# Performance work log

Hardware: AMD Instinct MI355X
Metric: run time of the kernel (lower is better)

The kernel has to match this reference:

```python
import jax, jax.numpy as jnp
import numpy as np

DIM = 1024
NUM_HEADS = 16
HEAD_DIM = DIM // NUM_HEADS
SCALE = HEAD_DIM ** -0.5


def setup_inputs() -> dict:
    key = jax.random.key(0)
    ks = jax.random.split(key, 10)
    B, N, C = 8, 2048, DIM
    std = C ** -0.5
    return {
        "query": jax.random.normal(ks[0], (B, N, C), jnp.float32),
        "key": jax.random.normal(ks[1], (B, N, C), jnp.float32),
        "value": jax.random.normal(ks[2], (B, N, C), jnp.float32),
        "xpos": jax.random.randint(ks[3], (B, N, 2), 0, 64),
        "ypos": jax.random.randint(ks[4], (B, N, 2), 0, 64),
        # Linear weights stored [out, in] like torch; qkv_bias=False so no q/k/v bias.
        "Wq": jax.random.normal(ks[5], (C, C), jnp.float32) * std,
        "Wk": jax.random.normal(ks[6], (C, C), jnp.float32) * std,
        "Wv": jax.random.normal(ks[7], (C, C), jnp.float32) * std,
        "Wp": jax.random.normal(ks[8], (C, C), jnp.float32) * std,
        "bp": jax.random.normal(ks[9], (C,), jnp.float32) * std,
    }


def reference(query, key, value, xpos, ypos, Wq, Wk, Wv, Wp, bp):
    B, N, C = query.shape
    H, D = NUM_HEADS, HEAD_DIM
    # Separate Q/K/V projections (no bias), reshape to (B, N, H, D).
    q = (query @ Wq.T).reshape(B, N, H, D)
    k = (key @ Wk.T).reshape(B, N, H, D)
    v = (value @ Wv.T).reshape(B, N, H, D)
    # rope is None in this config, so no rotary embedding is applied.
    # Faithful to the source: NO permute before q @ k^T, so the contraction is
    # over D with attention logits of shape (B, N, H, H) (softmax over heads).
    attn = jnp.einsum("bnhd,bngd->bnhg", q, k) * SCALE
    attn = jax.nn.softmax(attn, axis=-1)
    x = jnp.einsum("bnhg,bngd->bnhd", attn, v)  # (B, N, H, D)
    # torch: (attn @ v).transpose(1, 2).reshape(B, N, C)
    x = jnp.transpose(x, (0, 2, 1, 3)).reshape(B, N, C)
    # Output projection (has bias); dropouts are p=0 / eval -> identity.
    return x @ Wp.T + bp
```

## Files before the change

kernel.cpp:

```cpp
#include <hip/hip_runtime.h>
#include <stdint.h>

#define DEV __device__ __forceinline__

using f32x4 = __attribute__((ext_vector_type(4))) float;
using s16x8 = __attribute__((ext_vector_type(8))) short;

DEV uint16_t f2bf(float f) {
  union { float f; uint32_t u; } v; v.f = f;
  uint32_t r = v.u + 0x7fffu + ((v.u >> 16) & 1u);
  return (uint16_t)(r >> 16);
}
DEV uint32_t pack2(float a, float b) {
  return (uint32_t)f2bf(a) | ((uint32_t)f2bf(b) << 16);
}

DEV void gload_lds16(const void* g, void* l) {
  __builtin_amdgcn_global_load_lds(
      (__attribute__((address_space(1))) void*)(void*)g,
      (__attribute__((address_space(3))) void*)l, 16, 0, 0);
}

__global__ __launch_bounds__(256) void cvt_all_kernel(
    const float* __restrict__ q, const float* __restrict__ k,
    const float* __restrict__ v, const float* __restrict__ Wq,
    const float* __restrict__ Wk, const float* __restrict__ Wv,
    const float* __restrict__ Wp, uint16_t* __restrict__ qc,
    uint16_t* __restrict__ kc, uint16_t* __restrict__ vc,
    uint16_t* __restrict__ wqb, uint16_t* __restrict__ wkb,
    uint16_t* __restrict__ wvb, uint16_t* __restrict__ wpb) {
  const int idx = blockIdx.x * blockDim.x + threadIdx.x;
  const float* src;
  uint16_t* dst;
  int i;
  if (idx < 3 * 2097152) {
    const int t = idx >> 21;
    i = idx & 2097151;
    src = t == 0 ? q : t == 1 ? k : v;
    dst = t == 0 ? qc : t == 1 ? kc : vc;
  } else {
    const int j = idx - 3 * 2097152;
    const int r = j >> 17;
    i = j & 131071;
    src = r == 0 ? Wq : r == 1 ? Wk : r == 2 ? Wv : Wp;
    dst = r == 0 ? wqb : r == 1 ? wkb : r == 2 ? wvb : wpb;
  }
  const float4* s = (const float4*)src;
  float4 a = s[2 * i];
  float4 b = s[2 * i + 1];
  uint4 pk;
  pk.x = pack2(a.x, a.y);
  pk.y = pack2(a.z, a.w);
  pk.z = pack2(b.x, b.y);
  pk.w = pack2(b.z, b.w);
  ((uint4*)dst)[i] = pk;
}

struct GemmBatch {
  const uint16_t* A[3];
  const uint16_t* B[3];
  void* C[3];
};

template <bool OUT_BF16>
__global__ __launch_bounds__(512, 2) void gemm_bt256(GemmBatch gb,
                                                     const float* __restrict__ bias,
                                                     int M, int N, int K) {
  constexpr int BM = 256, BN = 256, BK = 32;
  __shared__ __align__(16) uint16_t Alds[4][BM * BK];
  __shared__ __align__(16) uint16_t Blds[4][BN * BK];

  const int w = blockIdx.x;
  const int xcd = w & 7;
  int local = w >> 3;
  const int nbn = N >> 8;
  const int bmpx = (M >> 8) >> 3;
  const int bn = local % nbn;
  local /= nbn;
  const int bml = local % bmpx;
  const int z = local / bmpx;
  const int bm0 = (xcd * bmpx + bml) * BM;
  const int bn0 = bn * BN;

  const uint16_t* __restrict__ Ap = gb.A[z];
  const uint16_t* __restrict__ Bp = gb.B[z];
  void* __restrict__ Cp = gb.C[z];

  const int tid = threadIdx.x;
  const int wave = tid >> 6;
  const int lane = tid & 63;
  const int quad = lane >> 4;
  const int l16 = lane & 15;
  const int wm = (wave >> 2) * 128;
  const int wn = (wave & 3) * 64;

  f32x4 acc[8][4];
#pragma unroll
  for (int i = 0; i < 8; ++i)
#pragma unroll
    for (int j = 0; j < 4; ++j) acc[i][j] = (f32x4){0.f, 0.f, 0.f, 0.f};

  const uint16_t* asrc[2];
  const uint16_t* bsrc[2];
  int sofs[2];
#pragma unroll
  for (int j = 0; j < 2; ++j) {
    const int p = wave * 128 + j * 64 + lane;
    const int m = p >> 2;
    const int c = p & 3;
    const int lc = c ^ ((m >> 1) & 3);
    asrc[j] = Ap + (size_t)(bm0 + m) * K + lc * 8;
    bsrc[j] = Bp + (size_t)(bn0 + m) * K + lc * 8;
    sofs[j] = (wave * 128 + j * 64) * 8;
  }

  const int NT = K >> 5;

#pragma unroll
  for (int tt = 0; tt < 3; ++tt) {
#pragma unroll
    for (int j = 0; j < 2; ++j) gload_lds16(asrc[j] + tt * BK, &Alds[tt][sofs[j]]);
#pragma unroll
    for (int j = 0; j < 2; ++j) gload_lds16(bsrc[j] + tt * BK, &Blds[tt][sofs[j]]);
  }

  for (int t = 0; t < NT; ++t) {
    const int buf = t & 3;
    if (t + 2 < NT) {
      asm volatile("s_waitcnt vmcnt(8)" ::: "memory");
    } else if (t + 1 < NT) {
      asm volatile("s_waitcnt vmcnt(4)" ::: "memory");
    } else {
      asm volatile("s_waitcnt vmcnt(0)" ::: "memory");
    }
    __builtin_amdgcn_s_barrier();
    __builtin_amdgcn_sched_barrier(0);

    if (t + 3 < NT) {
      const int sb = (t + 3) & 3;
      const int ko = (t + 3) * BK;
#pragma unroll
      for (int j = 0; j < 2; ++j) gload_lds16(asrc[j] + ko, &Alds[sb][sofs[j]]);
#pragma unroll
      for (int j = 0; j < 2; ++j) gload_lds16(bsrc[j] + ko, &Blds[sb][sofs[j]]);
    }

    s16x8 bf[4];
#pragma unroll
    for (int nf = 0; nf < 4; ++nf) {
      const int nl = wn + nf * 16 + l16;
      const int cb = nl * 4 + (quad ^ ((nl >> 1) & 3));
      bf[nf] = *(const s16x8*)&Blds[buf][cb * 8];
    }

#pragma unroll
    for (int ph = 0; ph < 4; ++ph) {
      const int ml0 = wm + (ph * 2) * 16 + l16;
      const int ca0 = ml0 * 4 + (quad ^ ((ml0 >> 1) & 3));
      s16x8 af0 = *(const s16x8*)&Alds[buf][ca0 * 8];
      const int ml1 = wm + (ph * 2 + 1) * 16 + l16;
      const int ca1 = ml1 * 4 + (quad ^ ((ml1 >> 1) & 3));
      s16x8 af1 = *(const s16x8*)&Alds[buf][ca1 * 8];
      __builtin_amdgcn_s_setprio(1);
#pragma unroll
      for (int nf = 0; nf < 4; ++nf) {
        acc[ph * 2][nf] =
            __builtin_amdgcn_mfma_f32_16x16x32_bf16(af0, bf[nf], acc[ph * 2][nf], 0, 0, 0);
        acc[ph * 2 + 1][nf] =
            __builtin_amdgcn_mfma_f32_16x16x32_bf16(af1, bf[nf], acc[ph * 2 + 1][nf], 0, 0, 0);
      }
      __builtin_amdgcn_s_setprio(0);
    }
  }

#pragma unroll
  for (int sm = 0; sm < 8; ++sm) {
    const int mrow = bm0 + wm + sm * 16 + quad * 4;
#pragma unroll
    for (int sn = 0; sn < 4; ++sn) {
      const int ncol = bn0 + wn + sn * 16 + l16;
      if constexpr (OUT_BF16) {
        uint16_t* Cb = (uint16_t*)Cp;
#pragma unroll
        for (int r = 0; r < 4; ++r) Cb[(size_t)(mrow + r) * N + ncol] = f2bf(acc[sm][sn][r]);
      } else {
        float* Cf = (float*)Cp;
        const float bv = bias[ncol];
#pragma unroll
        for (int r = 0; r < 4; ++r) Cf[(size_t)(mrow + r) * N + ncol] = acc[sm][sn][r] + bv;
      }
    }
  }
}

__global__ __launch_bounds__(256) void attn_kernel(const uint16_t* __restrict__ qb,
                                                   const uint16_t* __restrict__ kb,
                                                   const uint16_t* __restrict__ vb,
                                                   uint16_t* __restrict__ x2b) {
  __shared__ __align__(16) uint16_t plds[4][16 * 16];
  __shared__ __align__(16) uint16_t vlds[4][16 * 64];

  const int tid = threadIdx.x;
  const int wave = tid >> 6;
  const int lane = tid & 63;
  const int quad = lane >> 4;
  const int l16 = lane & 15;
  const int token = blockIdx.x * 4 + wave;
  const int b = token >> 11;
  const int n = token & 2047;
  const size_t base = (size_t)token * 1024;

  {
    const uint16_t* vt = vb + base;
    uint16_t* vl = vlds[wave];
#pragma unroll
    for (int c2 = 0; c2 < 2; ++c2) {
      const int p = lane + c2 * 64;
      const int g = p >> 3;
      const int cc = p & 7;
      const int cs = cc ^ (2 * (g >> 3));
      *(uint4*)&vl[g * 64 + cs * 8] = *(const uint4*)&vt[p * 8];
    }
  }

  const uint16_t* qrow = qb + base + l16 * 64 + quad * 8;
  const uint16_t* krow = kb + base + l16 * 64 + quad * 8;
  s16x8 aq0 = *(const s16x8*)qrow;
  s16x8 aq1 = *(const s16x8*)(qrow + 32);
  s16x8 bk0 = *(const s16x8*)krow;
  s16x8 bk1 = *(const s16x8*)(krow + 32);
  f32x4 s = (f32x4){0.f, 0.f, 0.f, 0.f};
  s = __builtin_amdgcn_mfma_f32_16x16x32_bf16(aq0, bk0, s, 0, 0, 0);
  s = __builtin_amdgcn_mfma_f32_16x16x32_bf16(aq1, bk1, s, 0, 0, 0);

  float p[4];
#pragma unroll
  for (int r = 0; r < 4; ++r) {
    float v = s[r] * 0.125f;
    float mx = v;
#pragma unroll
    for (int off = 1; off < 16; off <<= 1) mx = fmaxf(mx, __shfl_xor(mx, off));
    float e = __expf(v - mx);
    float sum = e;
#pragma unroll
    for (int off = 1; off < 16; off <<= 1) sum += __shfl_xor(sum, off);
    p[r] = e / sum;
  }

  uint16_t* pb = plds[wave];
#pragma unroll
  for (int r = 0; r < 4; ++r) pb[(quad * 4 + r) * 16 + l16] = f2bf(p[r]);
  __syncthreads();
  s16x8 ap = (s16x8){0, 0, 0, 0, 0, 0, 0, 0};
  if (quad < 2) ap = *(const s16x8*)&pb[l16 * 16 + quad * 8];

  s16x8 bv[4];
#pragma unroll
  for (int c = 0; c < 4; ++c) bv[c] = (s16x8){0, 0, 0, 0, 0, 0, 0, 0};
  if (quad < 2) {
    const uint16_t* vl = vlds[wave];
#pragma unroll
    for (int c = 0; c < 4; ++c) {
      const int cc = c * 2 + (l16 >> 3);
      const int dlo = l16 & 7;
#pragma unroll
      for (int j = 0; j < 8; ++j) {
        const int g = quad * 8 + j;
        const int cs = cc ^ (2 * (g >> 3));
        bv[c][j] = (short)vl[g * 64 + cs * 8 + dlo];
      }
    }
  }

  f32x4 xacc[4];
#pragma unroll
  for (int c = 0; c < 4; ++c) {
    xacc[c] = (f32x4){0.f, 0.f, 0.f, 0.f};
    xacc[c] = __builtin_amdgcn_mfma_f32_16x16x32_bf16(ap, bv[c], xacc[c], 0, 0, 0);
  }

  uint16_t* xout =
      x2b + (size_t)b * (2048 * 1024) + (size_t)(n & 15) * 64 + (size_t)(n >> 4) * 1024;
#pragma unroll
  for (int c = 0; c < 4; ++c) {
    const int d = c * 16 + l16;
#pragma unroll
    for (int r = 0; r < 4; ++r) {
      const int h = quad * 4 + r;
      xout[(size_t)h * 128 * 1024 + d] = f2bf(xacc[c][r]);
    }
  }
}

extern "C" void kernel_launch(void* const* d_in, const int* in_sizes, int n_in,
                              void* d_out, int out_size, void* d_ws, size_t ws_size,
                              hipStream_t stream) {
  const float* query = (const float*)d_in[0];
  const float* key = (const float*)d_in[1];
  const float* value = (const float*)d_in[2];
  const float* Wq = (const float*)d_in[5];
  const float* Wk = (const float*)d_in[6];
  const float* Wv = (const float*)d_in[7];
  const float* Wp = (const float*)d_in[8];
  const float* bp = (const float*)d_in[9];
  float* out = (float*)d_out;

  const int C = 1024;
  const int M = 8 * 2048;
  const size_t MC = (size_t)M * C;
  const size_t CC = (size_t)C * C;

  uint16_t* ws = (uint16_t*)d_ws;
  uint16_t* qb = ws;
  uint16_t* kb = qb + MC;
  uint16_t* vb = kb + MC;
  uint16_t* x2b = vb + MC;
  uint16_t* wqb = x2b + MC;
  uint16_t* wkb = wqb + CC;
  uint16_t* wvb = wkb + CC;
  uint16_t* wpb = wvb + CC;
  uint16_t* kin = wpb + CC;
  uint16_t* vin = kin + MC;
  uint16_t* qin = x2b;

  cvt_all_kernel<<<dim3(26624), dim3(256), 0, stream>>>(
      query, key, value, Wq, Wk, Wv, Wp, qin, kin, vin, wqb, wkb, wvb, wpb);

  GemmBatch qkv;
  qkv.A[0] = qin;  qkv.B[0] = wqb;  qkv.C[0] = qb;
  qkv.A[1] = kin;  qkv.B[1] = wkb;  qkv.C[1] = kb;
  qkv.A[2] = vin;  qkv.B[2] = wvb;  qkv.C[2] = vb;
  gemm_bt256<true><<<dim3((M / 256) * (C / 256) * 3), dim3(512), 0, stream>>>(
      qkv, nullptr, M, C, C);

  attn_kernel<<<dim3(M / 4), dim3(256), 0, stream>>>(qb, kb, vb, x2b);

  GemmBatch fin;
  fin.A[0] = x2b;  fin.B[0] = wpb;  fin.C[0] = out;
  fin.A[1] = x2b;  fin.B[1] = wpb;  fin.C[1] = out;
  fin.A[2] = x2b;  fin.B[2] = wpb;  fin.C[2] = out;
  gemm_bt256<false><<<dim3((M / 256) * (C / 256)), dim3(512), 0, stream>>>(fin, bp, M,
                                                                           C, C);
}
```

Measured before the change: 428.8 us.

## Restructure GEMM into BK=64 double-buffered eight-phase pipelined schedule

Replaces the 4-stage BK=32 GEMM mainloop with a double-buffered BK=64 loop. Each K tile is split into four sub-phases that interleave LDS fragment loads, global-to-LDS prefetch of half-tiles, and MFMA blocks, each phase bracketed by barriers. The aim is to overlap global loads, LDS reads and matrix math more finely and to halve the number of K iterations. In exchange it adds many more barriers per tile, and the larger tile (128KB of LDS) may limit occupancy under the requested two blocks per CU.

Measured after the change: 392.4 us. 8.5% less time.

```diff
diff --git a/kernel.cpp b/kernel.cpp
--- a/kernel.cpp
+++ b/kernel.cpp
@@ -63,12 +63,12 @@
 };
 
 template <bool OUT_BF16>
-__global__ __launch_bounds__(512, 2) void gemm_bt256(GemmBatch gb,
-                                                     const float* __restrict__ bias,
-                                                     int M, int N, int K) {
-  constexpr int BM = 256, BN = 256, BK = 32;
-  __shared__ __align__(16) uint16_t Alds[4][BM * BK];
-  __shared__ __align__(16) uint16_t Blds[4][BN * BK];
+__global__ __launch_bounds__(512, 2) void gemm8p(GemmBatch gb,
+                                                 const float* __restrict__ bias,
+                                                 int M, int N, int K) {
+  constexpr int BM = 256, BN = 256, BK = 64;
+  __shared__ __align__(16) uint16_t Alds[2][BM * BK];
+  __shared__ __align__(16) uint16_t Blds[2][BN * BK];
 
   const int w = blockIdx.x;
   const int xcd = w & 7;
@@ -100,77 +100,116 @@
 #pragma unroll
     for (int j = 0; j < 4; ++j) acc[i][j] = (f32x4){0.f, 0.f, 0.f, 0.f};
 
-  const uint16_t* asrc[2];
-  const uint16_t* bsrc[2];
-  int sofs[2];
-#pragma unroll
-  for (int j = 0; j < 2; ++j) {
-    const int p = wave * 128 + j * 64 + lane;
-    const int m = p >> 2;
-    const int c = p & 3;
-    const int lc = c ^ ((m >> 1) & 3);
-    asrc[j] = Ap + (size_t)(bm0 + m) * K + lc * 8;
-    bsrc[j] = Bp + (size_t)(bn0 + m) * K + lc * 8;
-    sofs[j] = (wave * 128 + j * 64) * 8;
-  }
-
-  const int NT = K >> 5;
-
-#pragma unroll
-  for (int tt = 0; tt < 3; ++tt) {
-#pragma unroll
-    for (int j = 0; j < 2; ++j) gload_lds16(asrc[j] + tt * BK, &Alds[tt][sofs[j]]);
-#pragma unroll
-    for (int j = 0; j < 2; ++j) gload_lds16(bsrc[j] + tt * BK, &Blds[tt][sofs[j]]);
-  }
-
-  for (int t = 0; t < NT; ++t) {
-    const int buf = t & 3;
-    if (t + 2 < NT) {
-      asm volatile("s_waitcnt vmcnt(8)" ::: "memory");
-    } else if (t + 1 < NT) {
-      asm volatile("s_waitcnt vmcnt(4)" ::: "memory");
-    } else {
-      asm volatile("s_waitcnt vmcnt(0)" ::: "memory");
-    }
+  size_t aofs[2][2], bofs[2][2];
+  int lofs[2][2];
+#pragma unroll
+  for (int h = 0; h < 2; ++h)
+#pragma unroll
+    for (int j = 0; j < 2; ++j) {
+      const int p = h * 1024 + wave * 128 + j * 64 + lane;
+      const int m = p >> 3;
+      const int lc = (p & 7) ^ ((m >> 1) & 7);
+      aofs[h][j] = (size_t)(bm0 + m) * K + lc * 8;
+      bofs[h][j] = (size_t)(bn0 + m) * K + lc * 8;
+      lofs[h][j] = (h * 1024 + wave * 128 + j * 64) * 8;
+    }
+
+  auto SA = [&](int tile, int h) {
+    uint16_t* base = Alds[tile & 1];
+#pragma unroll
+    for (int j = 0; j < 2; ++j)
+      gload_lds16(Ap + aofs[h][j] + (size_t)tile * BK, base + lofs[h][j]);
+  };
+  auto SB = [&](int tile, int h) {
+    uint16_t* base = Blds[tile & 1];
+#pragma unroll
+    for (int j = 0; j < 2; ++j)
+      gload_lds16(Bp + bofs[h][j] + (size_t)tile * BK, base + lofs[h][j]);
+  };
+
+  s16x8 Af[4][2], Bf[4][2];
+  auto LDA = [&](int buf, int mh) {
+#pragma unroll
+    for (int s = 0; s < 4; ++s) {
+      const int ml = wm + (mh * 4 + s) * 16 + l16;
+      const int sw = (ml >> 1) & 7;
+#pragma unroll
+      for (int k = 0; k < 2; ++k) {
+        const int cc = ml * 8 + ((k * 4 + quad) ^ sw);
+        Af[s][k] = *(const s16x8*)&Alds[buf][cc * 8];
+      }
+    }
+  };
+  auto LDB = [&](int buf, int nh) {
+#pragma unroll
+    for (int s = 0; s < 2; ++s) {
+      const int nl = wn + (nh * 2 + s) * 16 + l16;
+      const int sw = (nl >> 1) & 7;
+#pragma unroll
+      for (int k = 0; k < 2; ++k) {
+        const int cc = nl * 8 + ((k * 4 + quad) ^ sw);
+        Bf[nh * 2 + s][k] = *(const s16x8*)&Blds[buf][cc * 8];
+      }
+    }
+  };
+  auto OPEN = [&]() {
     __builtin_amdgcn_s_barrier();
+    asm volatile("s_waitcnt lgkmcnt(0)" ::: "memory");
     __builtin_amdgcn_sched_barrier(0);
-
-    if (t + 3 < NT) {
-      const int sb = (t + 3) & 3;
-      const int ko = (t + 3) * BK;
-#pragma unroll
-      for (int j = 0; j < 2; ++j) gload_lds16(asrc[j] + ko, &Alds[sb][sofs[j]]);
-#pragma unroll
-      for (int j = 0; j < 2; ++j) gload_lds16(bsrc[j] + ko, &Blds[sb][sofs[j]]);
-    }
-
-    s16x8 bf[4];
-#pragma unroll
-    for (int nf = 0; nf < 4; ++nf) {
-      const int nl = wn + nf * 16 + l16;
-      const int cb = nl * 4 + (quad ^ ((nl >> 1) & 3));
-      bf[nf] = *(const s16x8*)&Blds[buf][cb * 8];
-    }
-
-#pragma unroll
-    for (int ph = 0; ph < 4; ++ph) {
-      const int ml0 = wm + (ph * 2) * 16 + l16;
-      const int ca0 = ml0 * 4 + (quad ^ ((ml0 >> 1) & 3));
-      s16x8 af0 = *(const s16x8*)&Alds[buf][ca0 * 8];
-      const int ml1 = wm + (ph * 2 + 1) * 16 + l16;
-      const int ca1 = ml1 * 4 + (quad ^ ((ml1 >> 1) & 3));
-      s16x8 af1 = *(const s16x8*)&Alds[buf][ca1 * 8];
-      __builtin_amdgcn_s_setprio(1);
-#pragma unroll
-      for (int nf = 0; nf < 4; ++nf) {
-        acc[ph * 2][nf] =
-            __builtin_amdgcn_mfma_f32_16x16x32_bf16(af0, bf[nf], acc[ph * 2][nf], 0, 0, 0);
-        acc[ph * 2 + 1][nf] =
-            __builtin_amdgcn_mfma_f32_16x16x32_bf16(af1, bf[nf], acc[ph * 2 + 1][nf], 0, 0, 0);
-      }
-      __builtin_amdgcn_s_setprio(0);
-    }
+  };
+  auto MMA = [&](int mh, int nh) {
+    __builtin_amdgcn_s_setprio(1);
+#pragma unroll
+    for (int s = 0; s < 4; ++s)
+#pragma unroll
+      for (int n = 0; n < 2; ++n)
+#pragma unroll
+        for (int k = 0; k < 2; ++k)
+          acc[mh * 4 + s][nh * 2 + n] = __builtin_amdgcn_mfma_f32_16x16x32_bf16(
+              Af[s][k], Bf[nh * 2 + n][k], acc[mh * 4 + s][nh * 2 + n], 0, 0, 0);
+    __builtin_amdgcn_s_setprio(0);
+  };
+  auto CLOSE = [&]() { __builtin_amdgcn_s_barrier(); };
+
+  const int NT = K >> 6;
+  const int NI = NT >> 1;
+
+  SA(0, 0); SA(0, 1); SB(0, 0); SB(0, 1); SB(1, 0); SB(1, 1);
+  asm volatile("s_waitcnt vmcnt(4)" ::: "memory");
+  __builtin_amdgcn_s_barrier();
+
+  for (int i = 0; i < NI; ++i) {
+    const int t0 = 2 * i, t1 = 2 * i + 1;
+    const bool more = (t0 + 2 < NT);
+
+    LDA(0, 0); LDB(0, 0);
+    SA(t1, 0);
+    OPEN(); MMA(0, 0); CLOSE();
+    LDB(0, 1);
+    SA(t1, 1);
+    OPEN(); MMA(0, 1); CLOSE();
+    LDA(0, 1);
+    if (more) SB(t0 + 2, 0);
+    OPEN(); MMA(1, 0); CLOSE();
+    if (more) SB(t0 + 2, 1);
+    OPEN(); MMA(1, 1);
+    if (more) asm volatile("s_waitcnt vmcnt(4)" ::: "memory");
+    else      asm volatile("s_waitcnt vmcnt(0)" ::: "memory");
+    CLOSE();
+
+    LDA(1, 0); LDB(1, 0);
+    if (more) SA(t0 + 2, 0);
+    OPEN(); MMA(0, 0); CLOSE();
+    LDB(1, 1);
+    if (more) SA(t0 + 2, 1);
+    OPEN(); MMA(0, 1); CLOSE();
+    LDA(1, 1);
+    if (more) SB(t1 + 2, 0);
+    OPEN(); MMA(1, 0); CLOSE();
+    if (more) SB(t1 + 2, 1);
+    OPEN(); MMA(1, 1);
+    asm volatile("s_waitcnt vmcnt(4)" ::: "memory");
+    CLOSE();
   }
 
 #pragma unroll
@@ -330,8 +369,8 @@
   qkv.A[0] = qin;  qkv.B[0] = wqb;  qkv.C[0] = qb;
   qkv.A[1] = kin;  qkv.B[1] = wkb;  qkv.C[1] = kb;
   qkv.A[2] = vin;  qkv.B[2] = wvb;  qkv.C[2] = vb;
-  gemm_bt256<true><<<dim3((M / 256) * (C / 256) * 3), dim3(512), 0, stream>>>(
-      qkv, nullptr, M, C, C);
+  gemm8p<true><<<dim3((M / 256) * (C / 256) * 3), dim3(512), 0, stream>>>(qkv, nullptr,
+                                                                          M, C, C);
 
   attn_kernel<<<dim3(M / 4), dim3(256), 0, stream>>>(qb, kb, vb, x2b);
 
@@ -339,6 +378,5 @@
   fin.A[0] = x2b;  fin.B[0] = wpb;  fin.C[0] = out;
   fin.A[1] = x2b;  fin.B[1] = wpb;  fin.C[1] = out;
   fin.A[2] = x2b;  fin.B[2] = wpb;  fin.C[2] = out;
-  gemm_bt256<false><<<dim3((M / 256) * (C / 256)), dim3(512), 0, stream>>>(fin, bp, M,
-                                                                           C, C);
-}
+  gemm8p<false><<<dim3((M / 256) * (C / 256)), dim3(512), 0, stream>>>(fin, bp, M, C, C);
+}
```
